# Performance work log

Hardware: AMD Instinct MI355X
Metric: run time of the kernel (lower is better)

The kernel has to match this reference:

```python
import jax, jax.numpy as jnp
import numpy as np
import math

DIM = 1024
N_HEADS = 16
HEAD_DIM = DIM // N_HEADS
BS, SEQ, NNB = 8, 1024, 50
LN_EPS = 1e-12


def setup_inputs() -> dict:
    key = jax.random.key(0)
    ks = jax.random.split(key, 12)
    std = 0.02
    inp = {
        "x": jax.random.normal(ks[0], (BS, SEQ, DIM), jnp.float32),
        "x_neighbor": jax.random.normal(ks[1], (BS, NNB, DIM), jnp.float32),
        "mask": jnp.ones((BS, SEQ), jnp.int32),
        "neighbor_mask": jnp.ones((BS, NNB), jnp.float32),
        "qw": std * jax.random.normal(ks[2], (DIM, DIM), jnp.float32),
        "qb": jnp.zeros((DIM,), jnp.float32),
        "kw": std * jax.random.normal(ks[3], (DIM, DIM), jnp.float32),
        "kb": jnp.zeros((DIM,), jnp.float32),
        "vw": std * jax.random.normal(ks[4], (DIM, DIM), jnp.float32),
        "vb": jnp.zeros((DIM,), jnp.float32),
        "ow": std * jax.random.normal(ks[5], (DIM, DIM), jnp.float32),
        "ob": jnp.zeros((DIM,), jnp.float32),
        "ln_g": jnp.ones((DIM,), jnp.float32),
        "ln_b": jnp.zeros((DIM,), jnp.float32),
    }
    return inp


def _split_heads(t, bs):
    # [bs, s, dim] -> [bs, h, s, dh]
    return t.reshape(bs, -1, N_HEADS, HEAD_DIM).transpose(0, 2, 1, 3)


def reference(x, x_neighbor, mask, neighbor_mask, qw, qb, kw, kb, vw, vb, ow, ob, ln_g, ln_b):
    bs, seq, dim = x.shape
    # mean-pool neighbors with mask
    nm = neighbor_mask[..., None]                      # [bs, nnb, 1]
    xn = (x_neighbor * nm).sum(axis=1) / nm.sum(axis=1)  # [bs, dim]
    query = jnp.broadcast_to(xn[:, None, :], x.shape)    # [bs, seq, dim]

    q = _split_heads(query @ qw.T + qb, bs) / math.sqrt(HEAD_DIM)
    k = _split_heads(x @ kw.T + kb, bs)
    v = _split_heads(x @ vw.T + vb, bs)

    scores = jnp.einsum("bhqd,bhkd->bhqk", q, k)       # [bs, h, seq, seq]
    key_mask = (mask == 0)[:, None, None, :]            # [bs, 1, 1, seq]
    scores = jnp.where(key_mask, -jnp.inf, scores)
    weights = jax.nn.softmax(scores, axis=-1)           # dropout p=0.0 -> no-op
    context = jnp.einsum("bhqk,bhkd->bhqd", weights, v)
    context = context.transpose(0, 2, 1, 3).reshape(bs, seq, dim)
    out = context @ ow.T + ob

    h = out + x
    mu = h.mean(axis=-1, keepdims=True)
    var = ((h - mu) ** 2).mean(axis=-1, keepdims=True)
    return (h - mu) / jnp.sqrt(var + LN_EPS) * ln_g + ln_b
```

## Files before the change

### kernel.cpp

```cpp
#include <hip/hip_runtime.h>
#include <hip/hip_bf16.h>


#define DIM  1024
#define NH   16
#define HD   64
#define BS   8
#define SEQ  1024
#define NNB  50

__global__ void k_pool(const float* __restrict__ xnb, const float* __restrict__ nm,
                       float* __restrict__ xn){
  int b = blockIdx.x;
  int d = threadIdx.x*4;
  float4 acc = {0,0,0,0}; float wsum = 0.f;
  #pragma unroll 10
  for (int n=0; n<NNB; n++){
    float w = nm[b*NNB + n];
    float4 v = *(const float4*)(xnb + (size_t)(b*NNB + n)*DIM + d);
    acc.x += w*v.x; acc.y += w*v.y; acc.z += w*v.z; acc.w += w*v.w;
    wsum += w;
  }
  float inv = 1.f/wsum;
  acc.x*=inv; acc.y*=inv; acc.z*=inv; acc.w*=inv;
  *(float4*)(xn + b*DIM + d) = acc;
}

__global__ void k_q(const float* __restrict__ xn, const float* __restrict__ qw,
                    const float* __restrict__ qb, float* __restrict__ q){
  int wv = threadIdx.x >> 6, ln = threadIdx.x & 63;
  int j = blockIdx.x*4 + wv;
  float acc[BS] = {0,0,0,0,0,0,0,0};
  #pragma unroll
  for (int i=0; i<4; i++){
    int d = ln*4 + 256*i;
    float4 wt = *(const float4*)(qw + (size_t)j*DIM + d);
    #pragma unroll
    for (int b=0; b<BS; b++){
      float4 xv = *(const float4*)(xn + b*DIM + d);
      acc[b] += wt.x*xv.x + wt.y*xv.y + wt.z*xv.z + wt.w*xv.w;
    }
  }
  #pragma unroll
  for (int off=32; off>=1; off>>=1){
    #pragma unroll
    for (int b=0; b<BS; b++) acc[b] += __shfl_down(acc[b], off, 64);
  }
  if (ln == 0){
    float bias = qb[j];
    #pragma unroll
    for (int b=0; b<BS; b++) q[b*DIM + j] = (acc[b] + bias) * 0.125f;
  }
}

__global__ void k_p(const float* __restrict__ q, const float* __restrict__ kw,
                    float* __restrict__ p){
  int dc = blockIdx.x, h = blockIdx.y, b = blockIdx.z;
  int d = dc*256 + threadIdx.x;
  const float* qrow = q + b*DIM + h*HD;
  float acc = 0.f;
  #pragma unroll 8
  for (int j=0; j<HD; j++)
    acc += qrow[j] * kw[(size_t)(h*HD + j)*DIM + d];
  p[(size_t)(b*NH + h)*DIM + d] = acc;
}

__global__ void k_scores(const float* __restrict__ x, const float* __restrict__ p,
                         float* __restrict__ scp){
  int s0 = blockIdx.x * 64;
  int b  = blockIdx.y;
  int kc = blockIdx.z;
  int kbase = kc * 256;
  int tid = threadIdx.x;
  __shared__ float4 plds[256*5];
  __shared__ float  xlds[64*68];
  float* pf = (float*)plds;
  #pragma unroll
  for (int it=0; it<16; it++){
    int idx = it*256 + tid;
    int d = idx & 255, h = idx >> 8;
    pf[d*20 + h] = p[(size_t)(b*NH + h)*DIM + kbase + d];
  }
  int s = tid & 63, g = tid >> 6;
  float acc[4] = {0.f,0.f,0.f,0.f};
  for (int dk=0; dk<4; dk++){
    __syncthreads();
    #pragma unroll
    for (int it=0; it<4; it++){
      int idx = it*256 + tid;
      int dd4 = idx & 15, ss = idx >> 4;
      float4 v = *(const float4*)(x + (size_t)(b*SEQ + s0 + ss)*DIM + kbase + dk*64 + dd4*4);
      *(float4*)(xlds + ss*68 + dd4*4) = v;
    }
    __syncthreads();
    #pragma unroll 4
    for (int dd4=0; dd4<16; dd4++){
      float4 xq = *(const float4*)(xlds + s*68 + dd4*4);
      int dbase = (dk*64 + dd4*4)*5 + g;
      float4 p0 = plds[dbase], p1 = plds[dbase+5], p2 = plds[dbase+10], p3 = plds[dbase+15];
      acc[0] += xq.x*p0.x + xq.y*p1.x + xq.z*p2.x + xq.w*p3.x;
      acc[1] += xq.x*p0.y + xq.y*p1.y + xq.z*p2.y + xq.w*p3.y;
      acc[2] += xq.x*p0.z + xq.y*p1.z + xq.z*p2.z + xq.w*p3.z;
      acc[3] += xq.x*p0.w + xq.y*p1.w + xq.z*p2.w + xq.w*p3.w;
    }
  }
  float* slab = scp + (size_t)kc*(BS*NH*SEQ);
  #pragma unroll
  for (int u=0; u<4; u++)
    slab[(size_t)(b*NH + g*4 + u)*SEQ + s0 + s] = acc[u];
}

__global__ void k_softmax(float* __restrict__ scp, const int* __restrict__ mask){
  int b = blockIdx.x >> 4, h = blockIdx.x & 15;
  int tid = threadIdx.x;
  size_t rowoff = (size_t)(b*NH + h)*SEQ;
  float v[4];
  float mx = -3e38f;
  #pragma unroll
  for (int i=0; i<4; i++){
    int s = tid + 256*i;
    float v0 = 0.f;
    #pragma unroll
    for (int kc=0; kc<4; kc++) v0 += scp[(size_t)kc*(BS*NH*SEQ) + rowoff + s];
    if (mask[b*SEQ + s] == 0) v0 = -1e30f;
    v[i] = v0;
    mx = fmaxf(mx, v0);
  }
  #pragma unroll
  for (int off=32; off>=1; off>>=1) mx = fmaxf(mx, __shfl_xor(mx, off, 64));
  __shared__ float r1[4], r2[4];
  int wv = tid >> 6, ln = tid & 63;
  if (ln == 0) r1[wv] = mx;
  __syncthreads();
  mx = fmaxf(fmaxf(r1[0], r1[1]), fmaxf(r1[2], r1[3]));
  float sum = 0.f;
  #pragma unroll
  for (int i=0; i<4; i++){ v[i] = __expf(v[i] - mx); sum += v[i]; }
  #pragma unroll
  for (int off=32; off>=1; off>>=1) sum += __shfl_xor(sum, off, 64);
  if (ln == 0) r2[wv] = sum;
  __syncthreads();
  sum = r2[0] + r2[1] + r2[2] + r2[3];
  float inv = 1.f / sum;
  #pragma unroll
  for (int i=0; i<4; i++) scp[rowoff + tid + 256*i] = v[i] * inv;
}

__global__ void k_wpool(const float* __restrict__ x, const float* __restrict__ w,
                        float* __restrict__ xwp){
  int dc = blockIdx.x, b = blockIdx.y, scn = blockIdx.z;
  int tid = threadIdx.x;
  __shared__ float4 wlds[64*5];
  float* wf = (float*)wlds;
  #pragma unroll
  for (int it=0; it<4; it++){
    int idx = it*256 + tid;
    int ss = idx >> 4, hh = idx & 15;
    wf[ss*20 + hh] = w[(size_t)(b*NH + hh)*SEQ + scn*64 + ss];
  }
  __syncthreads();
  int ln = tid & 63, wv = tid >> 6;
  int d = dc*256 + ln*4;
  const float* xbase = x + (size_t)(b*SEQ + scn*64)*DIM + d;
  float4 a0={0,0,0,0}, a1={0,0,0,0}, a2={0,0,0,0}, a3={0,0,0,0};
  for (int sb=0; sb<64; sb+=8){
    float4 xq[8];
    #pragma unroll
    for (int u=0; u<8; u++)
      xq[u] = *(const float4*)(xbase + (size_t)(sb+u)*DIM);
    #pragma unroll
    for (int u=0; u<8; u++){
      float4 wq = wlds[(sb+u)*5 + wv];
      a0.x+=xq[u].x*wq.x; a0.y+=xq[u].y*wq.x; a0.z+=xq[u].z*wq.x; a0.w+=xq[u].w*wq.x;
      a1.x+=xq[u].x*wq.y; a1.y+=xq[u].y*wq.y; a1.z+=xq[u].z*wq.y; a1.w+=xq[u].w*wq.y;
      a2.x+=xq[u].x*wq.z; a2.y+=xq[u].y*wq.z; a2.z+=xq[u].z*wq.z; a2.w+=xq[u].w*wq.z;
      a3.x+=xq[u].x*wq.w; a3.y+=xq[u].y*wq.w; a3.z+=xq[u].z*wq.w; a3.w+=xq[u].w*wq.w;
    }
  }
  float* dst = xwp + (size_t)scn*(BS*NH*DIM) + (size_t)(b*NH + wv*4)*DIM + d;
  *(float4*)(dst          ) = a0;
  *(float4*)(dst +   DIM  ) = a1;
  *(float4*)(dst + 2*DIM  ) = a2;
  *(float4*)(dst + 3*DIM  ) = a3;
}

__global__ void k_xwred(const float* __restrict__ xwp, float* __restrict__ xw){
  int id = blockIdx.x*256 + threadIdx.x;
  float v = 0.f;
  #pragma unroll
  for (int scn=0; scn<16; scn++) v += xwp[(size_t)scn*(BS*NH*DIM) + id];
  xw[id] = v;
}

__global__ void k_ctx(const float* __restrict__ xw, const float* __restrict__ vw,
                      const float* __restrict__ vb, float* __restrict__ ctx){
  int wv = threadIdx.x >> 6, ln = threadIdx.x & 63;
  int jo = blockIdx.x*4 + wv;
  int h  = jo >> 6;
  float acc[BS] = {0,0,0,0,0,0,0,0};
  #pragma unroll
  for (int i=0; i<4; i++){
    int d = ln*4 + 256*i;
    float4 vv = *(const float4*)(vw + (size_t)jo*DIM + d);
    #pragma unroll
    for (int b=0; b<BS; b++){
      float4 xv = *(const float4*)(xw + (size_t)(b*NH + h)*DIM + d);
      acc[b] += vv.x*xv.x + vv.y*xv.y + vv.z*xv.z + vv.w*xv.w;
    }
  }
  #pragma unroll
  for (int off=32; off>=1; off>>=1){
    #pragma unroll
    for (int b=0; b<BS; b++) acc[b] += __shfl_down(acc[b], off, 64);
  }
  if (ln == 0){
    float bias = vb[jo];
    #pragma unroll
    for (int b=0; b<BS; b++) ctx[b*DIM + jo] = acc[b] + bias;
  }
}

__global__ void k_outrow(const float* __restrict__ ctx, const float* __restrict__ ow,
                         const float* __restrict__ ob, float* __restrict__ outr){
  int wv = threadIdx.x >> 6, ln = threadIdx.x & 63;
  int io = blockIdx.x*4 + wv;
  float acc[BS] = {0,0,0,0,0,0,0,0};
  #pragma unroll
  for (int i=0; i<4; i++){
    int d = ln*4 + 256*i;
    float4 wt = *(const float4*)(ow + (size_t)io*DIM + d);
    #pragma unroll
    for (int b=0; b<BS; b++){
      float4 cv = *(const float4*)(ctx + b*DIM + d);
      acc[b] += wt.x*cv.x + wt.y*cv.y + wt.z*cv.z + wt.w*cv.w;
    }
  }
  #pragma unroll
  for (int off=32; off>=1; off>>=1){
    #pragma unroll
    for (int b=0; b<BS; b++) acc[b] += __shfl_down(acc[b], off, 64);
  }
  if (ln == 0){
    float bias = ob[io];
    #pragma unroll
    for (int b=0; b<BS; b++) outr[b*DIM + io] = acc[b] + bias;
  }
}

__global__ void k_ln(const float* __restrict__ x, const float* __restrict__ outr,
                     const float* __restrict__ g, const float* __restrict__ bt,
                     float* __restrict__ out){
  int row = blockIdx.x;
  int b = row >> 10;
  size_t base = (size_t)row * DIM;
  int tid = threadIdx.x;
  float4 xv = ((const float4*)(x + base))[tid];
  float4 ov = ((const float4*)(outr + (size_t)b*DIM))[tid];
  float4 h;
  h.x = xv.x + ov.x; h.y = xv.y + ov.y; h.z = xv.z + ov.z; h.w = xv.w + ov.w;
  float s  = h.x + h.y + h.z + h.w;
  float s2 = h.x*h.x + h.y*h.y + h.z*h.z + h.w*h.w;
  #pragma unroll
  for (int off=32; off>=1; off>>=1){
    s  += __shfl_xor(s,  off, 64);
    s2 += __shfl_xor(s2, off, 64);
  }
  __shared__ float r1[4], r2[4];
  int wv = tid >> 6, ln = tid & 63;
  if (ln == 0){ r1[wv] = s; r2[wv] = s2; }
  __syncthreads();
  s  = r1[0] + r1[1] + r1[2] + r1[3];
  s2 = r2[0] + r2[1] + r2[2] + r2[3];
  float mu   = s  * (1.f/1024.f);
  float var  = s2 * (1.f/1024.f) - mu*mu;
  float rstd = rsqrtf(var + 1e-12f);
  float4 gv = ((const float4*)g)[tid];
  float4 bv = ((const float4*)bt)[tid];
  float4 y;
  y.x = (h.x - mu)*rstd*gv.x + bv.x;
  y.y = (h.y - mu)*rstd*gv.y + bv.y;
  y.z = (h.z - mu)*rstd*gv.z + bv.z;
  y.w = (h.w - mu)*rstd*gv.w + bv.w;
  ((float4*)(out + base))[tid] = y;
}

extern "C" void kernel_launch(void* const* d_in, const int* in_sizes, int n_in,
                              void* d_out, int out_size, void* d_ws, size_t ws_size,
                              hipStream_t stream) {
  const float* x    = (const float*)d_in[0];
  const float* xnb  = (const float*)d_in[1];
  const int*   mask = (const int*  )d_in[2];
  const float* nm   = (const float*)d_in[3];
  const float* qw   = (const float*)d_in[4];
  const float* qb   = (const float*)d_in[5];
  const float* kw   = (const float*)d_in[6];
  const float* vw   = (const float*)d_in[8];
  const float* vb   = (const float*)d_in[9];
  const float* ow   = (const float*)d_in[10];
  const float* ob   = (const float*)d_in[11];
  const float* lng  = (const float*)d_in[12];
  const float* lnb  = (const float*)d_in[13];
  float* out = (float*)d_out;

  float* ws   = (float*)d_ws;
  float* xn   = ws;
  float* q    = ws + 8192;
  float* p    = ws + 16384;
  float* scp  = ws + 147456;
  float* xwp  = ws + 671744;
  float* ctx  = ws + 2768896;
  float* outr = ws + 2777088;
  float* xw   = p;

  k_pool   <<<BS,              256, 0, stream>>>(xnb, nm, xn);
  k_q      <<<256,             256, 0, stream>>>(xn, qw, qb, q);
  k_p      <<<dim3(4,NH,BS),   256, 0, stream>>>(q, kw, p);
  k_scores <<<dim3(16,BS,4),   256, 0, stream>>>(x, p, scp);
  k_softmax<<<BS*NH,           256, 0, stream>>>(scp, mask);
  k_wpool  <<<dim3(4,BS,16),   256, 0, stream>>>(x, scp, xwp);
  k_xwred  <<<512,             256, 0, stream>>>(xwp, xw);
  k_ctx    <<<256,             256, 0, stream>>>(xw, vw, vb, ctx);
  k_outrow <<<256,             256, 0, stream>>>(ctx, ow, ob, outr);
  k_ln     <<<BS*SEQ,          256, 0, stream>>>(x, outr, lng, lnb, out);
}
```

Before: 170.6 us.

## Fuse nine stage kernels into one persistent kernel with grid-wide atomic barriers

Replaces the chain of nine dependent kernel launches after pooling with a single 512-block persistent kernel. The stages are separated by software grid barriers built on atomic counters, which a small prep kernel zeroes. The aim is to remove per-launch overhead and inter-kernel gaps, which matter because each stage does little work. The risks are deadlock if all 512 blocks are not co-resident (it relies on launch_bounds giving 2 blocks per CU), spin-wait cost at each barrier, and the layernorm stage now running 16 rows serially per block.

```diff
diff --git a/kernel.cpp b/kernel.cpp
--- a/kernel.cpp
+++ b/kernel.cpp
@@ -8,10 +8,22 @@
 #define BS   8
 #define SEQ  1024
 #define NNB  50
-
-__global__ void k_pool(const float* __restrict__ xnb, const float* __restrict__ nm,
-                       float* __restrict__ xn){
+#define NBLK 512u
+
+#define OF_XN    16
+#define OF_Q     8208
+#define OF_P     16400
+#define OF_SCP   147472
+#define OF_XWP   671760
+#define OF_XW    2768912
+#define OF_CTX   2899984
+#define OF_OUTR  2908176
+
+__global__ void k_prep(const float* __restrict__ xnb, const float* __restrict__ nm,
+                       float* __restrict__ ws){
   int b = blockIdx.x;
+  if (b == 0 && threadIdx.x < 16) ((unsigned*)ws)[threadIdx.x] = 0u;
+  float* xn = ws + OF_XN;
   int d = threadIdx.x*4;
   float4 acc = {0,0,0,0}; float wsum = 0.f;
   #pragma unroll 10
@@ -26,262 +38,294 @@
   *(float4*)(xn + b*DIM + d) = acc;
 }
 
-__global__ void k_q(const float* __restrict__ xn, const float* __restrict__ qw,
-                    const float* __restrict__ qb, float* __restrict__ q){
-  int wv = threadIdx.x >> 6, ln = threadIdx.x & 63;
-  int j = blockIdx.x*4 + wv;
-  float acc[BS] = {0,0,0,0,0,0,0,0};
-  #pragma unroll
-  for (int i=0; i<4; i++){
-    int d = ln*4 + 256*i;
-    float4 wt = *(const float4*)(qw + (size_t)j*DIM + d);
-    #pragma unroll
-    for (int b=0; b<BS; b++){
-      float4 xv = *(const float4*)(xn + b*DIM + d);
-      acc[b] += wt.x*xv.x + wt.y*xv.y + wt.z*xv.z + wt.w*xv.w;
-    }
-  }
-  #pragma unroll
-  for (int off=32; off>=1; off>>=1){
-    #pragma unroll
-    for (int b=0; b<BS; b++) acc[b] += __shfl_down(acc[b], off, 64);
-  }
-  if (ln == 0){
-    float bias = qb[j];
-    #pragma unroll
-    for (int b=0; b<BS; b++) q[b*DIM + j] = (acc[b] + bias) * 0.125f;
-  }
+__device__ __forceinline__ void gsync(unsigned* cnt, int slot){
+  __syncthreads();
+  if (threadIdx.x == 0){
+    __hip_atomic_fetch_add(cnt + slot, 1u, __ATOMIC_RELEASE, __HIP_MEMORY_SCOPE_AGENT);
+    while (__hip_atomic_load(cnt + slot, __ATOMIC_RELAXED, __HIP_MEMORY_SCOPE_AGENT) < NBLK){
+      __builtin_amdgcn_s_sleep(2);
+    }
+    __threadfence();
+  }
+  __syncthreads();
 }
 
-__global__ void k_p(const float* __restrict__ q, const float* __restrict__ kw,
-                    float* __restrict__ p){
-  int dc = blockIdx.x, h = blockIdx.y, b = blockIdx.z;
-  int d = dc*256 + threadIdx.x;
-  const float* qrow = q + b*DIM + h*HD;
-  float acc = 0.f;
-  #pragma unroll 8
-  for (int j=0; j<HD; j++)
-    acc += qrow[j] * kw[(size_t)(h*HD + j)*DIM + d];
-  p[(size_t)(b*NH + h)*DIM + d] = acc;
-}
-
-__global__ void k_scores(const float* __restrict__ x, const float* __restrict__ p,
-                         float* __restrict__ scp){
-  int s0 = blockIdx.x * 64;
-  int b  = blockIdx.y;
-  int kc = blockIdx.z;
-  int kbase = kc * 256;
+__global__ void __launch_bounds__(256, 2)
+k_mega(const float* __restrict__ x, const int* __restrict__ mask,
+       const float* __restrict__ qw, const float* __restrict__ qb,
+       const float* __restrict__ kw,
+       const float* __restrict__ vw, const float* __restrict__ vbias,
+       const float* __restrict__ ow, const float* __restrict__ obias,
+       const float* __restrict__ lng, const float* __restrict__ lnb,
+       float* __restrict__ ws, float* __restrict__ out)
+{
+  unsigned* cnt = (unsigned*)ws;
+  float* xn   = ws + OF_XN;
+  float* q    = ws + OF_Q;
+  float* p    = ws + OF_P;
+  float* scp  = ws + OF_SCP;
+  float* xwp  = ws + OF_XWP;
+  float* xw   = ws + OF_XW;
+  float* ctx  = ws + OF_CTX;
+  float* outr = ws + OF_OUTR;
+
+  __shared__ __align__(16) unsigned char smem[38912];
+  int vb  = blockIdx.x;
   int tid = threadIdx.x;
-  __shared__ float4 plds[256*5];
-  __shared__ float  xlds[64*68];
-  float* pf = (float*)plds;
-  #pragma unroll
-  for (int it=0; it<16; it++){
-    int idx = it*256 + tid;
-    int d = idx & 255, h = idx >> 8;
-    pf[d*20 + h] = p[(size_t)(b*NH + h)*DIM + kbase + d];
-  }
-  int s = tid & 63, g = tid >> 6;
-  float acc[4] = {0.f,0.f,0.f,0.f};
-  for (int dk=0; dk<4; dk++){
+  int wv  = tid >> 6, ln = tid & 63;
+
+  if (vb < 256){
+    int j = vb*4 + wv;
+    float acc[BS] = {0,0,0,0,0,0,0,0};
+    #pragma unroll
+    for (int i=0; i<4; i++){
+      int d = ln*4 + 256*i;
+      float4 wt = *(const float4*)(qw + (size_t)j*DIM + d);
+      #pragma unroll
+      for (int b=0; b<BS; b++){
+        float4 xv = *(const float4*)(xn + b*DIM + d);
+        acc[b] += wt.x*xv.x + wt.y*xv.y + wt.z*xv.z + wt.w*xv.w;
+      }
+    }
+    #pragma unroll
+    for (int off=32; off>=1; off>>=1){
+      #pragma unroll
+      for (int b=0; b<BS; b++) acc[b] += __shfl_down(acc[b], off, 64);
+    }
+    if (ln == 0){
+      float bias = qb[j];
+      #pragma unroll
+      for (int b=0; b<BS; b++) q[b*DIM + j] = (acc[b] + bias) * 0.125f;
+    }
+  }
+  gsync(cnt, 0);
+
+  {
+    int dc = vb & 3, h = (vb >> 2) & 15, b = vb >> 6;
+    int d = dc*256 + tid;
+    const float* qrow = q + b*DIM + h*HD;
+    float acc = 0.f;
+    #pragma unroll 8
+    for (int j=0; j<HD; j++)
+      acc += qrow[j] * kw[(size_t)(h*HD + j)*DIM + d];
+    p[(size_t)(b*NH + h)*DIM + d] = acc;
+  }
+  gsync(cnt, 1);
+
+  {
+    int s0 = (vb & 15) * 64;
+    int b  = (vb >> 4) & 7;
+    int kc = vb >> 7;
+    int kbase = kc * 256;
+    float4* plds = (float4*)smem;
+    float*  xlds = (float*)(smem + 20480);
+    float* pf = (float*)plds;
+    #pragma unroll
+    for (int it=0; it<16; it++){
+      int idx = it*256 + tid;
+      int d = idx & 255, h = idx >> 8;
+      pf[d*20 + h] = p[(size_t)(b*NH + h)*DIM + kbase + d];
+    }
+    int s = tid & 63, g = tid >> 6;
+    float acc[4] = {0.f,0.f,0.f,0.f};
+    for (int dk=0; dk<4; dk++){
+      __syncthreads();
+      #pragma unroll
+      for (int it=0; it<4; it++){
+        int idx = it*256 + tid;
+        int dd4 = idx & 15, ss = idx >> 4;
+        float4 v = *(const float4*)(x + (size_t)(b*SEQ + s0 + ss)*DIM + kbase + dk*64 + dd4*4);
+        *(float4*)(xlds + ss*68 + dd4*4) = v;
+      }
+      __syncthreads();
+      #pragma unroll 4
+      for (int dd4=0; dd4<16; dd4++){
+        float4 xq = *(const float4*)(xlds + s*68 + dd4*4);
+        int dbase = (dk*64 + dd4*4)*5 + g;
+        float4 p0 = plds[dbase], p1 = plds[dbase+5], p2 = plds[dbase+10], p3 = plds[dbase+15];
+        acc[0] += xq.x*p0.x + xq.y*p1.x + xq.z*p2.x + xq.w*p3.x;
+        acc[1] += xq.x*p0.y + xq.y*p1.y + xq.z*p2.y + xq.w*p3.y;
+        acc[2] += xq.x*p0.z + xq.y*p1.z + xq.z*p2.z + xq.w*p3.z;
+        acc[3] += xq.x*p0.w + xq.y*p1.w + xq.z*p2.w + xq.w*p3.w;
+      }
+    }
+    float* slab = scp + (size_t)kc*(BS*NH*SEQ);
+    #pragma unroll
+    for (int u=0; u<4; u++)
+      slab[(size_t)(b*NH + g*4 + u)*SEQ + s0 + s] = acc[u];
+  }
+  gsync(cnt, 2);
+
+  if (vb < 128){
+    int b = vb >> 4, h = vb & 15;
+    size_t rowoff = (size_t)(b*NH + h)*SEQ;
+    float* r1 = (float*)smem;
+    float* r2 = r1 + 4;
+    float v[4];
+    float mx = -3e38f;
+    #pragma unroll
+    for (int i=0; i<4; i++){
+      int s = tid + 256*i;
+      float v0 = 0.f;
+      #pragma unroll
+      for (int kc=0; kc<4; kc++) v0 += scp[(size_t)kc*(BS*NH*SEQ) + rowoff + s];
+      if (mask[b*SEQ + s] == 0) v0 = -1e30f;
+      v[i] = v0;
+      mx = fmaxf(mx, v0);
+    }
+    #pragma unroll
+    for (int off=32; off>=1; off>>=1) mx = fmaxf(mx, __shfl_xor(mx, off, 64));
+    if (ln == 0) r1[wv] = mx;
     __syncthreads();
+    mx = fmaxf(fmaxf(r1[0], r1[1]), fmaxf(r1[2], r1[3]));
+    float sum = 0.f;
+    #pragma unroll
+    for (int i=0; i<4; i++){ v[i] = __expf(v[i] - mx); sum += v[i]; }
+    #pragma unroll
+    for (int off=32; off>=1; off>>=1) sum += __shfl_xor(sum, off, 64);
+    if (ln == 0) r2[wv] = sum;
+    __syncthreads();
+    sum = r2[0] + r2[1] + r2[2] + r2[3];
+    float inv = 1.f / sum;
+    #pragma unroll
+    for (int i=0; i<4; i++) scp[rowoff + tid + 256*i] = v[i] * inv;
+  }
+  gsync(cnt, 3);
+
+  {
+    int dc = vb & 3, b = (vb >> 2) & 7, scn = vb >> 5;
+    float4* wlds = (float4*)smem;
+    float* wf = (float*)wlds;
     #pragma unroll
     for (int it=0; it<4; it++){
       int idx = it*256 + tid;
-      int dd4 = idx & 15, ss = idx >> 4;
-      float4 v = *(const float4*)(x + (size_t)(b*SEQ + s0 + ss)*DIM + kbase + dk*64 + dd4*4);
-      *(float4*)(xlds + ss*68 + dd4*4) = v;
+      int ss = idx >> 4, hh = idx & 15;
+      wf[ss*20 + hh] = scp[(size_t)(b*NH + hh)*SEQ + scn*64 + ss];
     }
     __syncthreads();
-    #pragma unroll 4
-    for (int dd4=0; dd4<16; dd4++){
-      float4 xq = *(const float4*)(xlds + s*68 + dd4*4);
-      int dbase = (dk*64 + dd4*4)*5 + g;
-      float4 p0 = plds[dbase], p1 = plds[dbase+5], p2 = plds[dbase+10], p3 = plds[dbase+15];
-      acc[0] += xq.x*p0.x + xq.y*p1.x + xq.z*p2.x + xq.w*p3.x;
-      acc[1] += xq.x*p0.y + xq.y*p1.y + xq.z*p2.y + xq.w*p3.y;
-      acc[2] += xq.x*p0.z + xq.y*p1.z + xq.z*p2.z + xq.w*p3.z;
-      acc[3] += xq.x*p0.w + xq.y*p1.w + xq.z*p2.w + xq.w*p3.w;
-    }
-  }
-  float* slab = scp + (size_t)kc*(BS*NH*SEQ);
-  #pragma unroll
-  for (int u=0; u<4; u++)
-    slab[(size_t)(b*NH + g*4 + u)*SEQ + s0 + s] = acc[u];
-}
-
-__global__ void k_softmax(float* __restrict__ scp, const int* __restrict__ mask){
-  int b = blockIdx.x >> 4, h = blockIdx.x & 15;
-  int tid = threadIdx.x;
-  size_t rowoff = (size_t)(b*NH + h)*SEQ;
-  float v[4];
-  float mx = -3e38f;
-  #pragma unroll
-  for (int i=0; i<4; i++){
-    int s = tid + 256*i;
-    float v0 = 0.f;
-    #pragma unroll
-    for (int kc=0; kc<4; kc++) v0 += scp[(size_t)kc*(BS*NH*SEQ) + rowoff + s];
-    if (mask[b*SEQ + s] == 0) v0 = -1e30f;
-    v[i] = v0;
-    mx = fmaxf(mx, v0);
-  }
-  #pragma unroll
-  for (int off=32; off>=1; off>>=1) mx = fmaxf(mx, __shfl_xor(mx, off, 64));
-  __shared__ float r1[4], r2[4];
-  int wv = tid >> 6, ln = tid & 63;
-  if (ln == 0) r1[wv] = mx;
-  __syncthreads();
-  mx = fmaxf(fmaxf(r1[0], r1[1]), fmaxf(r1[2], r1[3]));
-  float sum = 0.f;
-  #pragma unroll
-  for (int i=0; i<4; i++){ v[i] = __expf(v[i] - mx); sum += v[i]; }
-  #pragma unroll
-  for (int off=32; off>=1; off>>=1) sum += __shfl_xor(sum, off, 64);
-  if (ln == 0) r2[wv] = sum;
-  __syncthreads();
-  sum = r2[0] + r2[1] + r2[2] + r2[3];
-  float inv = 1.f / sum;
-  #pragma unroll
-  for (int i=0; i<4; i++) scp[rowoff + tid + 256*i] = v[i] * inv;
-}
-
-__global__ void k_wpool(const float* __restrict__ x, const float* __restrict__ w,
-                        float* __restrict__ xwp){
-  int dc = blockIdx.x, b = blockIdx.y, scn = blockIdx.z;
-  int tid = threadIdx.x;
-  __shared__ float4 wlds[64*5];
-  float* wf = (float*)wlds;
-  #pragma unroll
-  for (int it=0; it<4; it++){
-    int idx = it*256 + tid;
-    int ss = idx >> 4, hh = idx & 15;
-    wf[ss*20 + hh] = w[(size_t)(b*NH + hh)*SEQ + scn*64 + ss];
-  }
-  __syncthreads();
-  int ln = tid & 63, wv = tid >> 6;
-  int d = dc*256 + ln*4;
-  const float* xbase = x + (size_t)(b*SEQ + scn*64)*DIM + d;
-  float4 a0={0,0,0,0}, a1={0,0,0,0}, a2={0,0,0,0}, a3={0,0,0,0};
-  for (int sb=0; sb<64; sb+=8){
-    float4 xq[8];
-    #pragma unroll
-    for (int u=0; u<8; u++)
-      xq[u] = *(const float4*)(xbase + (size_t)(sb+u)*DIM);
-    #pragma unroll
-    for (int u=0; u<8; u++){
-      float4 wq = wlds[(sb+u)*5 + wv];
-      a0.x+=xq[u].x*wq.x; a0.y+=xq[u].y*wq.x; a0.z+=xq[u].z*wq.x; a0.w+=xq[u].w*wq.x;
-      a1.x+=xq[u].x*wq.y; a1.y+=xq[u].y*wq.y; a1.z+=xq[u].z*wq.y; a1.w+=xq[u].w*wq.y;
-      a2.x+=xq[u].x*wq.z; a2.y+=xq[u].y*wq.z; a2.z+=xq[u].z*wq.z; a2.w+=xq[u].w*wq.z;
-      a3.x+=xq[u].x*wq.w; a3.y+=xq[u].y*wq.w; a3.z+=xq[u].z*wq.w; a3.w+=xq[u].w*wq.w;
-    }
-  }
-  float* dst = xwp + (size_t)scn*(BS*NH*DIM) + (size_t)(b*NH + wv*4)*DIM + d;
-  *(float4*)(dst          ) = a0;
-  *(float4*)(dst +   DIM  ) = a1;
-  *(float4*)(dst + 2*DIM  ) = a2;
-  *(float4*)(dst + 3*DIM  ) = a3;
-}
-
-__global__ void k_xwred(const float* __restrict__ xwp, float* __restrict__ xw){
-  int id = blockIdx.x*256 + threadIdx.x;
-  float v = 0.f;
-  #pragma unroll
-  for (int scn=0; scn<16; scn++) v += xwp[(size_t)scn*(BS*NH*DIM) + id];
-  xw[id] = v;
-}
-
-__global__ void k_ctx(const float* __restrict__ xw, const float* __restrict__ vw,
-                      const float* __restrict__ vb, float* __restrict__ ctx){
-  int wv = threadIdx.x >> 6, ln = threadIdx.x & 63;
-  int jo = blockIdx.x*4 + wv;
-  int h  = jo >> 6;
-  float acc[BS] = {0,0,0,0,0,0,0,0};
-  #pragma unroll
-  for (int i=0; i<4; i++){
-    int d = ln*4 + 256*i;
-    float4 vv = *(const float4*)(vw + (size_t)jo*DIM + d);
-    #pragma unroll
-    for (int b=0; b<BS; b++){
-      float4 xv = *(const float4*)(xw + (size_t)(b*NH + h)*DIM + d);
-      acc[b] += vv.x*xv.x + vv.y*xv.y + vv.z*xv.z + vv.w*xv.w;
-    }
-  }
-  #pragma unroll
-  for (int off=32; off>=1; off>>=1){
-    #pragma unroll
-    for (int b=0; b<BS; b++) acc[b] += __shfl_down(acc[b], off, 64);
-  }
-  if (ln == 0){
-    float bias = vb[jo];
-    #pragma unroll
-    for (int b=0; b<BS; b++) ctx[b*DIM + jo] = acc[b] + bias;
-  }
-}
-
-__global__ void k_outrow(const float* __restrict__ ctx, const float* __restrict__ ow,
-                         const float* __restrict__ ob, float* __restrict__ outr){
-  int wv = threadIdx.x >> 6, ln = threadIdx.x & 63;
-  int io = blockIdx.x*4 + wv;
-  float acc[BS] = {0,0,0,0,0,0,0,0};
-  #pragma unroll
-  for (int i=0; i<4; i++){
-    int d = ln*4 + 256*i;
-    float4 wt = *(const float4*)(ow + (size_t)io*DIM + d);
-    #pragma unroll
-    for (int b=0; b<BS; b++){
-      float4 cv = *(const float4*)(ctx + b*DIM + d);
-      acc[b] += wt.x*cv.x + wt.y*cv.y + wt.z*cv.z + wt.w*cv.w;
-    }
-  }
-  #pragma unroll
-  for (int off=32; off>=1; off>>=1){
-    #pragma unroll
-    for (int b=0; b<BS; b++) acc[b] += __shfl_down(acc[b], off, 64);
-  }
-  if (ln == 0){
-    float bias = ob[io];
-    #pragma unroll
-    for (int b=0; b<BS; b++) outr[b*DIM + io] = acc[b] + bias;
-  }
-}
-
-__global__ void k_ln(const float* __restrict__ x, const float* __restrict__ outr,
-                     const float* __restrict__ g, const float* __restrict__ bt,
-                     float* __restrict__ out){
-  int row = blockIdx.x;
-  int b = row >> 10;
-  size_t base = (size_t)row * DIM;
-  int tid = threadIdx.x;
-  float4 xv = ((const float4*)(x + base))[tid];
-  float4 ov = ((const float4*)(outr + (size_t)b*DIM))[tid];
-  float4 h;
-  h.x = xv.x + ov.x; h.y = xv.y + ov.y; h.z = xv.z + ov.z; h.w = xv.w + ov.w;
-  float s  = h.x + h.y + h.z + h.w;
-  float s2 = h.x*h.x + h.y*h.y + h.z*h.z + h.w*h.w;
-  #pragma unroll
-  for (int off=32; off>=1; off>>=1){
-    s  += __shfl_xor(s,  off, 64);
-    s2 += __shfl_xor(s2, off, 64);
-  }
-  __shared__ float r1[4], r2[4];
-  int wv = tid >> 6, ln = tid & 63;
-  if (ln == 0){ r1[wv] = s; r2[wv] = s2; }
-  __syncthreads();
-  s  = r1[0] + r1[1] + r1[2] + r1[3];
-  s2 = r2[0] + r2[1] + r2[2] + r2[3];
-  float mu   = s  * (1.f/1024.f);
-  float var  = s2 * (1.f/1024.f) - mu*mu;
-  float rstd = rsqrtf(var + 1e-12f);
-  float4 gv = ((const float4*)g)[tid];
-  float4 bv = ((const float4*)bt)[tid];
-  float4 y;
-  y.x = (h.x - mu)*rstd*gv.x + bv.x;
-  y.y = (h.y - mu)*rstd*gv.y + bv.y;
-  y.z = (h.z - mu)*rstd*gv.z + bv.z;
-  y.w = (h.w - mu)*rstd*gv.w + bv.w;
-  ((float4*)(out + base))[tid] = y;
+    int d = dc*256 + ln*4;
+    const float* xbase = x + (size_t)(b*SEQ + scn*64)*DIM + d;
+    float4 a0={0,0,0,0}, a1={0,0,0,0}, a2={0,0,0,0}, a3={0,0,0,0};
+    for (int sb=0; sb<64; sb+=8){
+      float4 xq[8];
+      #pragma unroll
+      for (int u=0; u<8; u++)
+        xq[u] = *(const float4*)(xbase + (size_t)(sb+u)*DIM);
+      #pragma unroll
+      for (int u=0; u<8; u++){
+        float4 wq = wlds[(sb+u)*5 + wv];
+        a0.x+=xq[u].x*wq.x; a0.y+=xq[u].y*wq.x; a0.z+=xq[u].z*wq.x; a0.w+=xq[u].w*wq.x;
+        a1.x+=xq[u].x*wq.y; a1.y+=xq[u].y*wq.y; a1.z+=xq[u].z*wq.y; a1.w+=xq[u].w*wq.y;
+        a2.x+=xq[u].x*wq.z; a2.y+=xq[u].y*wq.z; a2.z+=xq[u].z*wq.z; a2.w+=xq[u].w*wq.z;
+        a3.x+=xq[u].x*wq.w; a3.y+=xq[u].y*wq.w; a3.z+=xq[u].z*wq.w; a3.w+=xq[u].w*wq.w;
+      }
+    }
+    float* dst = xwp + (size_t)scn*(BS*NH*DIM) + (size_t)(b*NH + wv*4)*DIM + d;
+    *(float4*)(dst                 ) = a0;
+    *(float4*)(dst +   (size_t)DIM ) = a1;
+    *(float4*)(dst + 2*(size_t)DIM ) = a2;
+    *(float4*)(dst + 3*(size_t)DIM ) = a3;
+  }
+  gsync(cnt, 4);
+
+  {
+    int id = vb*256 + tid;
+    float v = 0.f;
+    #pragma unroll
+    for (int scn=0; scn<16; scn++) v += xwp[(size_t)scn*(BS*NH*DIM) + id];
+    xw[id] = v;
+  }
+  gsync(cnt, 5);
+
+  if (vb < 256){
+    int jo = vb*4 + wv;
+    int h  = jo >> 6;
+    float acc[BS] = {0,0,0,0,0,0,0,0};
+    #pragma unroll
+    for (int i=0; i<4; i++){
+      int d = ln*4 + 256*i;
+      float4 vv = *(const float4*)(vw + (size_t)jo*DIM + d);
+      #pragma unroll
+      for (int b=0; b<BS; b++){
+        float4 xv = *(const float4*)(xw + (size_t)(b*NH + h)*DIM + d);
+        acc[b] += vv.x*xv.x + vv.y*xv.y + vv.z*xv.z + vv.w*xv.w;
+      }
+    }
+    #pragma unroll
+    for (int off=32; off>=1; off>>=1){
+      #pragma unroll
+      for (int b=0; b<BS; b++) acc[b] += __shfl_down(acc[b], off, 64);
+    }
+    if (ln == 0){
+      float bias = vbias[jo];
+      #pragma unroll
+      for (int b=0; b<BS; b++) ctx[b*DIM + jo] = acc[b] + bias;
+    }
+  }
+  gsync(cnt, 6);
+
+  if (vb < 256){
+    int io = vb*4 + wv;
+    float acc[BS] = {0,0,0,0,0,0,0,0};
+    #pragma unroll
+    for (int i=0; i<4; i++){
+      int d = ln*4 + 256*i;
+      float4 wt = *(const float4*)(ow + (size_t)io*DIM + d);
+      #pragma unroll
+      for (int b=0; b<BS; b++){
+        float4 cv = *(const float4*)(ctx + b*DIM + d);
+        acc[b] += wt.x*cv.x + wt.y*cv.y + wt.z*cv.z + wt.w*cv.w;
+      }
+    }
+    #pragma unroll
+    for (int off=32; off>=1; off>>=1){
+      #pragma unroll
+      for (int b=0; b<BS; b++) acc[b] += __shfl_down(acc[b], off, 64);
+    }
+    if (ln == 0){
+      float bias = obias[io];
+      #pragma unroll
+      for (int b=0; b<BS; b++) outr[b*DIM + io] = acc[b] + bias;
+    }
+  }
+  gsync(cnt, 7);
+
+  {
+    float* r1 = (float*)smem;
+    float* r2 = r1 + 4;
+    for (int r=0; r<16; r++){
+      int row = vb*16 + r;
+      int b = row >> 10;
+      size_t base = (size_t)row * DIM;
+      float4 xv = ((const float4*)(x + base))[tid];
+      float4 ov = ((const float4*)(outr + (size_t)b*DIM))[tid];
+      float4 h;
+      h.x = xv.x + ov.x; h.y = xv.y + ov.y; h.z = xv.z + ov.z; h.w = xv.w + ov.w;
+      float s  = h.x + h.y + h.z + h.w;
+      float s2 = h.x*h.x + h.y*h.y + h.z*h.z + h.w*h.w;
+      #pragma unroll
+      for (int off=32; off>=1; off>>=1){
+        s  += __shfl_xor(s,  off, 64);
+        s2 += __shfl_xor(s2, off, 64);
+      }
+      if (ln == 0){ r1[wv] = s; r2[wv] = s2; }
+      __syncthreads();
+      s  = r1[0] + r1[1] + r1[2] + r1[3];
+      s2 = r2[0] + r2[1] + r2[2] + r2[3];
+      float mu   = s  * (1.f/1024.f);
+      float var  = s2 * (1.f/1024.f) - mu*mu;
+      float rstd = rsqrtf(var + 1e-12f);
+      float4 gv = ((const float4*)lng)[tid];
+      float4 bv = ((const float4*)lnb)[tid];
+      float4 y;
+      y.x = (h.x - mu)*rstd*gv.x + bv.x;
+      y.y = (h.y - mu)*rstd*gv.y + bv.y;
+      y.z = (h.z - mu)*rstd*gv.z + bv.z;
+      y.w = (h.w - mu)*rstd*gv.w + bv.w;
+      ((float4*)(out + base))[tid] = y;
+      __syncthreads();
+    }
+  }
 }
 
 extern "C" void kernel_launch(void* const* d_in, const int* in_sizes, int n_in,
@@ -301,25 +345,9 @@
   const float* lng  = (const float*)d_in[12];
   const float* lnb  = (const float*)d_in[13];
   float* out = (float*)d_out;
-
-  float* ws   = (float*)d_ws;
-  float* xn   = ws;
-  float* q    = ws + 8192;
-  float* p    = ws + 16384;
-  float* scp  = ws + 147456;
-  float* xwp  = ws + 671744;
-  float* ctx  = ws + 2768896;
-  float* outr = ws + 2777088;
-  float* xw   = p;
-
-  k_pool   <<<BS,              256, 0, stream>>>(xnb, nm, xn);
-  k_q      <<<256,             256, 0, stream>>>(xn, qw, qb, q);
-  k_p      <<<dim3(4,NH,BS),   256, 0, stream>>>(q, kw, p);
-  k_scores <<<dim3(16,BS,4),   256, 0, stream>>>(x, p, scp);
-  k_softmax<<<BS*NH,           256, 0, stream>>>(scp, mask);
-  k_wpool  <<<dim3(4,BS,16),   256, 0, stream>>>(x, scp, xwp);
-  k_xwred  <<<512,             256, 0, stream>>>(xwp, xw);
-  k_ctx    <<<256,             256, 0, stream>>>(xw, vw, vb, ctx);
-  k_outrow <<<256,             256, 0, stream>>>(ctx, ow, ob, outr);
-  k_ln     <<<BS*SEQ,          256, 0, stream>>>(x, outr, lng, lnb, out);
+  float* ws  = (float*)d_ws;
+
+  k_prep <<<BS,   256, 0, stream>>>(xnb, nm, ws);
+  k_mega <<<NBLK, 256, 0, stream>>>(x, mask, qw, qb, kw, vw, vb, ow, ob,
+                                    lng, lnb, ws, out);
 }
```

New measurement: 486.8 us. +185.3%, slower.

## Fuse query prep kernels and fold softmax normalization into weighted-pool reduction

Applied to the files above, without the earlier changes.

Neighbor pooling, the query projection and the key-projected query are merged into one kernel with one block per (batch, head), so two launches and their global round trips go away. Each block recomputes the pooled vector and reads its own head's query-weight rows, so there is redundant pooling work and repeated query-weight reads across batches. The separate softmax kernel is removed. The weighted-pool kernel now sums the score partials, applies the mask and exponentiates, and also emits per-chunk denominators. The final reduction divides numerator by denominator. Dropping the max subtraction can overflow for large scores.

```diff
diff --git a/kernel.cpp b/kernel.cpp
--- a/kernel.cpp
+++ b/kernel.cpp
@@ -9,60 +9,66 @@
 #define SEQ  1024
 #define NNB  50
 
-__global__ void k_pool(const float* __restrict__ xnb, const float* __restrict__ nm,
-                       float* __restrict__ xn){
-  int b = blockIdx.x;
-  int d = threadIdx.x*4;
-  float4 acc = {0,0,0,0}; float wsum = 0.f;
-  #pragma unroll 10
-  for (int n=0; n<NNB; n++){
-    float w = nm[b*NNB + n];
-    float4 v = *(const float4*)(xnb + (size_t)(b*NNB + n)*DIM + d);
-    acc.x += w*v.x; acc.y += w*v.y; acc.z += w*v.z; acc.w += w*v.w;
-    wsum += w;
-  }
-  float inv = 1.f/wsum;
-  acc.x*=inv; acc.y*=inv; acc.z*=inv; acc.w*=inv;
-  *(float4*)(xn + b*DIM + d) = acc;
-}
-
-__global__ void k_q(const float* __restrict__ xn, const float* __restrict__ qw,
-                    const float* __restrict__ qb, float* __restrict__ q){
-  int wv = threadIdx.x >> 6, ln = threadIdx.x & 63;
-  int j = blockIdx.x*4 + wv;
-  float acc[BS] = {0,0,0,0,0,0,0,0};
-  #pragma unroll
-  for (int i=0; i<4; i++){
-    int d = ln*4 + 256*i;
-    float4 wt = *(const float4*)(qw + (size_t)j*DIM + d);
-    #pragma unroll
-    for (int b=0; b<BS; b++){
-      float4 xv = *(const float4*)(xn + b*DIM + d);
-      acc[b] += wt.x*xv.x + wt.y*xv.y + wt.z*xv.z + wt.w*xv.w;
-    }
-  }
-  #pragma unroll
-  for (int off=32; off>=1; off>>=1){
-    #pragma unroll
-    for (int b=0; b<BS; b++) acc[b] += __shfl_down(acc[b], off, 64);
-  }
-  if (ln == 0){
-    float bias = qb[j];
-    #pragma unroll
-    for (int b=0; b<BS; b++) q[b*DIM + j] = (acc[b] + bias) * 0.125f;
-  }
-}
-
-__global__ void k_p(const float* __restrict__ q, const float* __restrict__ kw,
-                    float* __restrict__ p){
-  int dc = blockIdx.x, h = blockIdx.y, b = blockIdx.z;
-  int d = dc*256 + threadIdx.x;
-  const float* qrow = q + b*DIM + h*HD;
-  float acc = 0.f;
-  #pragma unroll 8
-  for (int j=0; j<HD; j++)
-    acc += qrow[j] * kw[(size_t)(h*HD + j)*DIM + d];
-  p[(size_t)(b*NH + h)*DIM + d] = acc;
+#define OF_P     16
+#define OF_SCP   131088
+#define OF_NUMP  655376
+#define OF_DENP  2752528
+#define OF_XW    2754576
+#define OF_CTX   2885648
+#define OF_OUTR  2893840
+
+__global__ void k_prep(const float* __restrict__ xnb, const float* __restrict__ nm,
+                       const float* __restrict__ qw, const float* __restrict__ qb,
+                       const float* __restrict__ kw, float* __restrict__ p){
+  int h = blockIdx.x & 15, b = blockIdx.x >> 4;
+  int tid = threadIdx.x, wv = tid >> 6, ln = tid & 63;
+  __shared__ float xnl[1024];
+  __shared__ float qp[256];
+  __shared__ float ql[64];
+  {
+    int d = tid*4;
+    float4 acc = {0,0,0,0}; float wsum = 0.f;
+    #pragma unroll 10
+    for (int n=0; n<NNB; n++){
+      float w = nm[b*NNB + n];
+      float4 v = *(const float4*)(xnb + (size_t)(b*NNB + n)*DIM + d);
+      acc.x += w*v.x; acc.y += w*v.y; acc.z += w*v.z; acc.w += w*v.w;
+      wsum += w;
+    }
+    float inv = 1.f/wsum;
+    acc.x*=inv; acc.y*=inv; acc.z*=inv; acc.w*=inv;
+    *(float4*)(xnl + d) = acc;
+  }
+  __syncthreads();
+  {
+    const float* qrow = qw + (size_t)(h*HD + ln)*DIM + wv*256;
+    const float* xrow = xnl + wv*256;
+    float part = 0.f;
+    #pragma unroll 16
+    for (int i=0; i<64; i++){
+      float4 a = *(const float4*)(qrow + i*4);
+      float4 c = *(const float4*)(xrow + i*4);
+      part += a.x*c.x + a.y*c.y + a.z*c.z + a.w*c.w;
+    }
+    qp[wv*64 + ln] = part;
+  }
+  __syncthreads();
+  if (wv == 0){
+    float qv = qp[ln] + qp[64+ln] + qp[128+ln] + qp[192+ln];
+    ql[ln] = (qv + qb[h*HD + ln]) * 0.125f;
+  }
+  __syncthreads();
+  {
+    int d = tid*4;
+    float4 acc = {0,0,0,0};
+    #pragma unroll 8
+    for (int j=0; j<HD; j++){
+      float qj = ql[j];
+      float4 kv = *(const float4*)(kw + (size_t)(h*HD + j)*DIM + d);
+      acc.x += qj*kv.x; acc.y += qj*kv.y; acc.z += qj*kv.z; acc.w += qj*kv.w;
+    }
+    *(float4*)(p + (size_t)(b*NH + h)*DIM + d) = acc;
+  }
 }
 
 __global__ void k_scores(const float* __restrict__ x, const float* __restrict__ p,
@@ -110,44 +116,9 @@
     slab[(size_t)(b*NH + g*4 + u)*SEQ + s0 + s] = acc[u];
 }
 
-__global__ void k_softmax(float* __restrict__ scp, const int* __restrict__ mask){
-  int b = blockIdx.x >> 4, h = blockIdx.x & 15;
-  int tid = threadIdx.x;
-  size_t rowoff = (size_t)(b*NH + h)*SEQ;
-  float v[4];
-  float mx = -3e38f;
-  #pragma unroll
-  for (int i=0; i<4; i++){
-    int s = tid + 256*i;
-    float v0 = 0.f;
-    #pragma unroll
-    for (int kc=0; kc<4; kc++) v0 += scp[(size_t)kc*(BS*NH*SEQ) + rowoff + s];
-    if (mask[b*SEQ + s] == 0) v0 = -1e30f;
-    v[i] = v0;
-    mx = fmaxf(mx, v0);
-  }
-  #pragma unroll
-  for (int off=32; off>=1; off>>=1) mx = fmaxf(mx, __shfl_xor(mx, off, 64));
-  __shared__ float r1[4], r2[4];
-  int wv = tid >> 6, ln = tid & 63;
-  if (ln == 0) r1[wv] = mx;
-  __syncthreads();
-  mx = fmaxf(fmaxf(r1[0], r1[1]), fmaxf(r1[2], r1[3]));
-  float sum = 0.f;
-  #pragma unroll
-  for (int i=0; i<4; i++){ v[i] = __expf(v[i] - mx); sum += v[i]; }
-  #pragma unroll
-  for (int off=32; off>=1; off>>=1) sum += __shfl_xor(sum, off, 64);
-  if (ln == 0) r2[wv] = sum;
-  __syncthreads();
-  sum = r2[0] + r2[1] + r2[2] + r2[3];
-  float inv = 1.f / sum;
-  #pragma unroll
-  for (int i=0; i<4; i++) scp[rowoff + tid + 256*i] = v[i] * inv;
-}
-
-__global__ void k_wpool(const float* __restrict__ x, const float* __restrict__ w,
-                        float* __restrict__ xwp){
+__global__ void k_wpe(const float* __restrict__ x, const float* __restrict__ scp,
+                      const int* __restrict__ mask,
+                      float* __restrict__ nump, float* __restrict__ denp){
   int dc = blockIdx.x, b = blockIdx.y, scn = blockIdx.z;
   int tid = threadIdx.x;
   __shared__ float4 wlds[64*5];
@@ -156,9 +127,20 @@
   for (int it=0; it<4; it++){
     int idx = it*256 + tid;
     int ss = idx >> 4, hh = idx & 15;
-    wf[ss*20 + hh] = w[(size_t)(b*NH + hh)*SEQ + scn*64 + ss];
-  }
-  __syncthreads();
+    int s  = scn*64 + ss;
+    float sc = 0.f;
+    #pragma unroll
+    for (int kc=0; kc<4; kc++)
+      sc += scp[(size_t)kc*(BS*NH*SEQ) + (size_t)(b*NH + hh)*SEQ + s];
+    wf[ss*20 + hh] = mask[b*SEQ + s] ? __expf(sc) : 0.f;
+  }
+  __syncthreads();
+  if (dc == 0 && tid < 16){
+    float dsum = 0.f;
+    #pragma unroll 16
+    for (int ss=0; ss<64; ss++) dsum += wf[ss*20 + tid];
+    denp[(scn*BS + b)*NH + tid] = dsum;
+  }
   int ln = tid & 63, wv = tid >> 6;
   int d = dc*256 + ln*4;
   const float* xbase = x + (size_t)(b*SEQ + scn*64)*DIM + d;
@@ -177,19 +159,25 @@
       a3.x+=xq[u].x*wq.w; a3.y+=xq[u].y*wq.w; a3.z+=xq[u].z*wq.w; a3.w+=xq[u].w*wq.w;
     }
   }
-  float* dst = xwp + (size_t)scn*(BS*NH*DIM) + (size_t)(b*NH + wv*4)*DIM + d;
-  *(float4*)(dst          ) = a0;
-  *(float4*)(dst +   DIM  ) = a1;
-  *(float4*)(dst + 2*DIM  ) = a2;
-  *(float4*)(dst + 3*DIM  ) = a3;
-}
-
-__global__ void k_xwred(const float* __restrict__ xwp, float* __restrict__ xw){
+  float* dst = nump + (size_t)scn*(BS*NH*DIM) + (size_t)(b*NH + wv*4)*DIM + d;
+  *(float4*)(dst                 ) = a0;
+  *(float4*)(dst +   (size_t)DIM ) = a1;
+  *(float4*)(dst + 2*(size_t)DIM ) = a2;
+  *(float4*)(dst + 3*(size_t)DIM ) = a3;
+}
+
+__global__ void k_xwred(const float* __restrict__ nump, const float* __restrict__ denp,
+                        float* __restrict__ xw){
   int id = blockIdx.x*256 + threadIdx.x;
-  float v = 0.f;
-  #pragma unroll
-  for (int scn=0; scn<16; scn++) v += xwp[(size_t)scn*(BS*NH*DIM) + id];
-  xw[id] = v;
+  int bh = id >> 10;
+  int b = bh >> 4, h = bh & 15;
+  float den = 0.f;
+  #pragma unroll
+  for (int scn=0; scn<16; scn++) den += denp[(scn*BS + b)*NH + h];
+  float num = 0.f;
+  #pragma unroll
+  for (int scn=0; scn<16; scn++) num += nump[(size_t)scn*(BS*NH*DIM) + id];
+  xw[id] = num / den;
 }
 
 __global__ void k_ctx(const float* __restrict__ xw, const float* __restrict__ vw,
@@ -303,23 +291,19 @@
   float* out = (float*)d_out;
 
   float* ws   = (float*)d_ws;
-  float* xn   = ws;
-  float* q    = ws + 8192;
-  float* p    = ws + 16384;
-  float* scp  = ws + 147456;
-  float* xwp  = ws + 671744;
-  float* ctx  = ws + 2768896;
-  float* outr = ws + 2777088;
-  float* xw   = p;
-
-  k_pool   <<<BS,              256, 0, stream>>>(xnb, nm, xn);
-  k_q      <<<256,             256, 0, stream>>>(xn, qw, qb, q);
-  k_p      <<<dim3(4,NH,BS),   256, 0, stream>>>(q, kw, p);
-  k_scores <<<dim3(16,BS,4),   256, 0, stream>>>(x, p, scp);
-  k_softmax<<<BS*NH,           256, 0, stream>>>(scp, mask);
-  k_wpool  <<<dim3(4,BS,16),   256, 0, stream>>>(x, scp, xwp);
-  k_xwred  <<<512,             256, 0, stream>>>(xwp, xw);
-  k_ctx    <<<256,             256, 0, stream>>>(xw, vw, vb, ctx);
-  k_outrow <<<256,             256, 0, stream>>>(ctx, ow, ob, outr);
-  k_ln     <<<BS*SEQ,          256, 0, stream>>>(x, outr, lng, lnb, out);
-}
+  float* p    = ws + OF_P;
+  float* scp  = ws + OF_SCP;
+  float* nump = ws + OF_NUMP;
+  float* denp = ws + OF_DENP;
+  float* xw   = ws + OF_XW;
+  float* ctx  = ws + OF_CTX;
+  float* outr = ws + OF_OUTR;
+
+  k_prep  <<<128,             256, 0, stream>>>(xnb, nm, qw, qb, kw, p);
+  k_scores<<<dim3(16,BS,4),   256, 0, stream>>>(x, p, scp);
+  k_wpe   <<<dim3(4,BS,16),   256, 0, stream>>>(x, scp, mask, nump, denp);
+  k_xwred <<<512,             256, 0, stream>>>(nump, denp, xw);
+  k_ctx   <<<256,             256, 0, stream>>>(xw, vw, vb, ctx);
+  k_outrow<<<256,             256, 0, stream>>>(ctx, ow, ob, outr);
+  k_ln    <<<BS*SEQ,          256, 0, stream>>>(x, outr, lng, lnb, out);
+}
```

New measurement: 168.3 us. Within noise of the previous version (-1.4%).
